# Kernel optimization log

Hardware: AMD Instinct MI355X
Metric: run time of the kernel (lower is better)

The kernel has to match this reference:

```python
import jax, jax.numpy as jnp
import numpy as np

B = 2048
D = 40960          # util.half_kp_numel(): 64 king squares * 640 piece-square planes
BASE = 288
MOVE = 4096        # util.move_numel(): 64 from-squares * 64 to-squares
MOVE_SIZE = (64, 64)


def setup_inputs() -> dict:
    key = jax.random.key(0)
    ks = jax.random.split(key, 24)
    f32 = jnp.float32
    # forward args: sparse one-hot half-kp occupancy vectors (modeled as rand floats)
    pov = (jax.random.uniform(ks[0], (B, 1), f32) > 0.5).astype(f32)
    white = (jax.random.uniform(ks[1], (B, D), f32) < 0.001).astype(f32)
    black = (jax.random.uniform(ks[2], (B, D), f32) < 0.001).astype(f32)
    s = 0.01
    p = {
        'W_w': jax.random.normal(ks[3], (BASE, D), f32) * s,
        'b_w': jnp.zeros((BASE,), f32),
        'W_b': jax.random.normal(ks[4], (BASE, D), f32) * s,
        'b_b': jnp.zeros((BASE,), f32),
        'W_v0': jax.random.normal(ks[5], (32, 2 * BASE), f32) * s,
        'b_v0': jnp.zeros((32,), f32),
        'W_v1': jax.random.normal(ks[6], (32, 32), f32) * s,
        'b_v1': jnp.zeros((32,), f32),
        'W_v2': jax.random.normal(ks[7], (1, 32), f32) * s,
        'b_v2': jnp.zeros((1,), f32),
        'W_a0': jax.random.normal(ks[8], (144, 2 * BASE), f32) * s,
        'b_a0': jnp.zeros((144,), f32),
        'W_a1': jax.random.normal(ks[9], (MOVE, 144), f32) * s,
        'b_a1': jnp.zeros((MOVE,), f32),
        'W_vs': jax.random.normal(ks[10], (1, 2 * BASE), f32) * s,
        'b_vs': jnp.zeros((1,), f32),
        'W_as': jax.random.normal(ks[11], (MOVE, 2 * BASE), f32) * s,
        'b_as': jnp.zeros((MOVE,), f32),
    }
    return dict(pov=pov, white=white, black=black, **p)


def _linear(x, W, b):
    return x @ W.T + b


def reference(pov, white, black, W_w, b_w, W_b, b_b,
              W_v0, b_v0, W_v1, b_v1, W_v2, b_v2,
              W_a0, b_a0, W_a1, b_a1, W_vs, b_vs, W_as, b_as):
    # half-kp affine accumulators (the sparse gather-sum candidate)
    w256 = _linear(white, W_w, b_w)            # [B, BASE]
    b256 = _linear(black, W_b, b_b)            # [B, BASE]
    cat_wb = jnp.concatenate([w256, b256], axis=1)
    cat_bw = jnp.concatenate([b256, w256], axis=1)
    base = jax.nn.relu(pov * cat_wb + (1.0 - pov) * cat_bw)  # [B, 2*BASE]
    # value head with skip
    val = jax.nn.relu(_linear(base, W_v0, b_v0))
    val = jax.nn.relu(_linear(val, W_v1, b_v1))
    val = _linear(val, W_v2, b_v2) + _linear(base, W_vs, b_vs)   # [B, 1]
    # action head with skip
    act = jax.nn.relu(_linear(base, W_a0, b_a0))
    act = _linear(act, W_a1, b_a1) + _linear(base, W_as, b_as)   # [B, MOVE]
    act = act.reshape(act.shape[0], *MOVE_SIZE)                  # [B, 64, 64]
    return (val, act)
```

## Files before the change

### kernel.cpp

```cpp
#include <hip/hip_runtime.h>

#define D_IN 40960
#define NB 2048
#define BASEN 288
#define CAPL 95
#define LSTRIDE 96
#define KP 736

typedef __attribute__((ext_vector_type(4))) float f32x4;
typedef __attribute__((ext_vector_type(8))) short short8;

__device__ inline float bf2f(ushort u) {
    unsigned v = ((unsigned)u) << 16; float f; __builtin_memcpy(&f, &v, 4); return f;
}
__device__ inline ushort f2bf(float f) {
    unsigned x; __builtin_memcpy(&x, &f, 4);
    unsigned r = (x + 0x7FFFu + ((x >> 16) & 1u)) >> 16; return (ushort)r;
}

__device__ inline void llds16(const void* g, void* l) {
    __builtin_amdgcn_global_load_lds((const __attribute__((address_space(1))) unsigned*)g,
                                     (__attribute__((address_space(3))) unsigned*)l, 16, 0, 0);
}

__global__ __launch_bounds__(256) void scan_kernel(const float* __restrict__ white,
                                                   const float* __restrict__ black,
                                                   int* __restrict__ lists) {
    int b = blockIdx.x, c = blockIdx.y;
    const float* src = (c ? black : white) + (size_t)b * D_IN;
    __shared__ int cnt;
    __shared__ int idxs[CAPL];
    if (threadIdx.x == 0) cnt = 0;
    __syncthreads();
    const uint4* v = (const uint4*)src;
    for (int it = 0; it < D_IN / (256 * 4); ++it) {
        int vi = it * 256 + threadIdx.x;
        uint4 x = v[vi];
        unsigned wds[4] = {x.x, x.y, x.z, x.w};
#pragma unroll
        for (int q = 0; q < 4; ++q) {
            if (wds[q]) { int p = atomicAdd(&cnt, 1); if (p < CAPL) idxs[p] = vi * 4 + q; }
        }
    }
    __syncthreads();
    int n = min(cnt, CAPL);
    int* dst = lists + ((size_t)c * NB + b) * LSTRIDE;
    if (threadIdx.x == 0) dst[0] = n;
    for (int i = threadIdx.x; i < n; i += 256) dst[1 + i] = idxs[i];
}

__global__ __launch_bounds__(256) void transpose_kernel(const float* __restrict__ src,
                                                        ushort* __restrict__ dst) {
    __shared__ float tile[32][65];
    int i = threadIdx.x;
    int d0 = blockIdx.x * 64, o0 = blockIdx.y * 32;
    int tr = i >> 4, tc4 = (i & 15) * 4;
#pragma unroll
    for (int rep = 0; rep < 2; ++rep) {
        int row = tr + rep * 16;
        float4 u = *(const float4*)&src[(size_t)(o0 + row) * D_IN + d0 + tc4];
        tile[row][tc4] = u.x; tile[row][tc4 + 1] = u.y; tile[row][tc4 + 2] = u.z; tile[row][tc4 + 3] = u.w;
    }
    __syncthreads();
    int dr = i >> 3, oc4 = (i & 7) * 4;
#pragma unroll
    for (int rep = 0; rep < 2; ++rep) {
        int d = dr + rep * 32;
        ushort4 u;
        u.x = f2bf(tile[oc4][d]); u.y = f2bf(tile[oc4 + 1][d]);
        u.z = f2bf(tile[oc4 + 2][d]); u.w = f2bf(tile[oc4 + 3][d]);
        *(ushort4*)&dst[(size_t)(d0 + d) * BASEN + o0 + oc4] = u;
    }
}

__global__ __launch_bounds__(288) void gatherW_kernel(const int* __restrict__ lists,
                                                      const ushort* __restrict__ Wt,
                                                      const float* __restrict__ b_w,
                                                      float* __restrict__ accW) {
    int b = blockIdx.x, t = threadIdx.x;
    __shared__ int idx[CAPL];
    __shared__ int ncnt;
    const int* lw = lists + (size_t)b * LSTRIDE;
    if (t == 0) ncnt = min(lw[0], CAPL);
    for (int i = t; i < CAPL; i += 288) idx[i] = lw[1 + i];
    __syncthreads();
    float acc = b_w[t];
    int n = ncnt;
#pragma unroll 4
    for (int i = 0; i < n; ++i) acc += bf2f(Wt[(size_t)idx[i] * BASEN + t]);
    accW[(size_t)b * BASEN + t] = acc;
}

__global__ __launch_bounds__(288) void gatherB_kernel(const int* __restrict__ lists,
                                                      const ushort* __restrict__ Wt,
                                                      const float* __restrict__ accW,
                                                      const float* __restrict__ pov,
                                                      const float* __restrict__ b_b,
                                                      const float* __restrict__ W_a0,
                                                      const float* __restrict__ b_a0,
                                                      ushort* __restrict__ hidden) {
    int b = blockIdx.x, t = threadIdx.x;
    __shared__ int idx[CAPL];
    __shared__ int ncnt;
    __shared__ float baseS[576];
    const int* lb = lists + ((size_t)NB + b) * LSTRIDE;
    if (t == 0) ncnt = min(lb[0], CAPL);
    for (int i = t; i < CAPL; i += 288) idx[i] = lb[1 + i];
    __syncthreads();
    float accB = b_b[t];
    int n = ncnt;
#pragma unroll 4
    for (int i = 0; i < n; ++i) accB += bf2f(Wt[(size_t)idx[i] * BASEN + t]);
    float aW = accW[(size_t)b * BASEN + t];
    float p = pov[b];
    float b0 = fmaxf(p * aW + (1.0f - p) * accB, 0.0f);
    float b1 = fmaxf(p * accB + (1.0f - p) * aW, 0.0f);
    baseS[t] = b0; baseS[288 + t] = b1;
    ushort* hrow = hidden + (size_t)b * KP;
    hrow[160 + t] = f2bf(b0);
    hrow[160 + 288 + t] = f2bf(b1);
    if (t < 16) hrow[144 + t] = 0;
    __syncthreads();
    int o = t >> 1, half = t & 1;
    const float* wrow = W_a0 + (size_t)o * 576 + half * 288;
    const float* bp = &baseS[half * 288];
    float s = 0.f;
#pragma unroll
    for (int j = 0; j < 288; j += 4) {
        float4 q = *(const float4*)(wrow + j);
        s += bp[j + 0] * q.x + bp[j + 1] * q.y + bp[j + 2] * q.z + bp[j + 3] * q.w;
    }
    s += __shfl_xor(s, 1);
    if (half == 0) hrow[o] = f2bf(fmaxf(s + b_a0[o], 0.f));
}

__global__ __launch_bounds__(256) void wcat_kernel(const float* __restrict__ W_a1,
                                                   const float* __restrict__ W_as,
                                                   const float* __restrict__ b_a1,
                                                   const float* __restrict__ b_as,
                                                   ushort* __restrict__ Wcat,
                                                   float* __restrict__ biasA) {
    int m = blockIdx.x, t = threadIdx.x;
    ushort* dst = Wcat + (size_t)m * KP;
    if (t < 144) dst[t] = f2bf(W_a1[(size_t)m * 144 + t]);
    if (t >= 144 && t < 160) dst[t] = 0;
    for (int j = t; j < 576; j += 256) dst[160 + j] = f2bf(W_as[(size_t)m * 576 + j]);
    if (t == 200) biasA[m] = b_a1[m] + b_as[m];
}

__global__ __launch_bounds__(64) void val_kernel(const ushort* __restrict__ hidden,
                                                 const float* __restrict__ W_v0, const float* __restrict__ b_v0,
                                                 const float* __restrict__ W_v1, const float* __restrict__ b_v1,
                                                 const float* __restrict__ W_v2, const float* __restrict__ b_v2,
                                                 const float* __restrict__ W_vs, const float* __restrict__ b_vs,
                                                 float* __restrict__ outv) {
    int b = blockIdx.x, t = threadIdx.x;
    __shared__ float bl[576];
    __shared__ float v0s[32];
    __shared__ float skipS;
    const ushort* hrow = hidden + (size_t)b * KP + 160;
    for (int i = t; i < 576; i += 64) bl[i] = bf2f(hrow[i]);
    __syncthreads();
    if (t < 32) {
        float s = b_v0[t];
        const float* w = W_v0 + (size_t)t * 576;
        for (int j = 0; j < 576; ++j) s += bl[j] * w[j];
        v0s[t] = fmaxf(s, 0.f);
    } else {
        int u = t - 32;
        float s = 0.f;
        for (int j = u; j < 576; j += 32) s += bl[j] * W_vs[j];
        s += __shfl_xor(s, 1); s += __shfl_xor(s, 2); s += __shfl_xor(s, 4);
        s += __shfl_xor(s, 8); s += __shfl_xor(s, 16);
        if (u == 0) skipS = s;
    }
    __syncthreads();
    if (t < 32) {
        float s = b_v1[t];
        const float* w = W_v1 + (size_t)t * 32;
        for (int j = 0; j < 32; ++j) s += v0s[j] * w[j];
        float v1t = fmaxf(s, 0.f);
        float part = v1t * W_v2[t];
        part += __shfl_xor(part, 1); part += __shfl_xor(part, 2); part += __shfl_xor(part, 4);
        part += __shfl_xor(part, 8); part += __shfl_xor(part, 16);
        if (t == 0) outv[b] = part + b_v2[0] + skipS + b_vs[0];
    }
}

__global__ __launch_bounds__(256) void gemm_act(const ushort* __restrict__ A,
                                                const ushort* __restrict__ Bm,
                                                const float* __restrict__ biasA,
                                                float* __restrict__ outa) {
    __shared__ ushort As[128 * 32];
    __shared__ ushort Bs[128 * 32];
    int tid = threadIdx.x;
    int lane = tid & 63, wv = tid >> 6;
    int bm = blockIdx.x, bn = blockIdx.y;
    int wm = wv & 1, wn = wv >> 1;
    f32x4 acc[4][4];
#pragma unroll
    for (int mt = 0; mt < 4; ++mt)
#pragma unroll
        for (int nt = 0; nt < 4; ++nt) { f32x4 z = {0.f, 0.f, 0.f, 0.f}; acc[mt][nt] = z; }

    int r = tid >> 2, c8 = (tid & 3) * 8;
    const ushort* Ag = A  + (size_t)(bm * 128 + r) * KP + c8;
    const ushort* Bg = Bm + (size_t)(bn * 128 + r) * KP + c8;
    ushort* AsW = As + wv * 512;
    ushort* BsW = Bs + wv * 512;

    int kg = (lane >> 4) * 8;
    int rA = wm * 64 + (lane & 15);
    int rB = wn * 64 + (lane & 15);

    for (int kk = 0; kk < KP; kk += 32) {
        llds16(Ag + kk, AsW);
        llds16(Ag + (size_t)64 * KP + kk, AsW + 2048);
        llds16(Bg + kk, BsW);
        llds16(Bg + (size_t)64 * KP + kk, BsW + 2048);
        __syncthreads();
        short8 af[4], bf[4];
#pragma unroll
        for (int mt = 0; mt < 4; ++mt) af[mt] = *(const short8*)&As[(rA + mt * 16) * 32 + kg];
#pragma unroll
        for (int nt = 0; nt < 4; ++nt) bf[nt] = *(const short8*)&Bs[(rB + nt * 16) * 32 + kg];
#pragma unroll
        for (int mt = 0; mt < 4; ++mt)
#pragma unroll
            for (int nt = 0; nt < 4; ++nt)
                acc[mt][nt] = __builtin_amdgcn_mfma_f32_16x16x32_bf16(af[mt], bf[nt], acc[mt][nt], 0, 0, 0);
        __syncthreads();
    }

    int colb = bn * 128 + wn * 64 + (lane & 15);
    int rowb = bm * 128 + wm * 64 + ((lane >> 4) << 2);
#pragma unroll
    for (int nt = 0; nt < 4; ++nt) {
        float bia = biasA[colb + nt * 16];
#pragma unroll
        for (int mt = 0; mt < 4; ++mt) {
#pragma unroll
            for (int q = 0; q < 4; ++q) {
                int rr = rowb + mt * 16 + q;
                outa[(size_t)rr * 4096 + colb + nt * 16] = acc[mt][nt][q] + bia;
            }
        }
    }
}

extern "C" void kernel_launch(void* const* d_in, const int* in_sizes, int n_in,
                              void* d_out, int out_size, void* d_ws, size_t ws_size,
                              hipStream_t stream) {
    const float* pov   = (const float*)d_in[0];
    const float* white = (const float*)d_in[1];
    const float* black = (const float*)d_in[2];
    const float* W_w   = (const float*)d_in[3];
    const float* b_w   = (const float*)d_in[4];
    const float* W_b   = (const float*)d_in[5];
    const float* b_b   = (const float*)d_in[6];
    const float* W_v0  = (const float*)d_in[7];
    const float* b_v0  = (const float*)d_in[8];
    const float* W_v1  = (const float*)d_in[9];
    const float* b_v1  = (const float*)d_in[10];
    const float* W_v2  = (const float*)d_in[11];
    const float* b_v2  = (const float*)d_in[12];
    const float* W_a0  = (const float*)d_in[13];
    const float* b_a0  = (const float*)d_in[14];
    const float* W_a1  = (const float*)d_in[15];
    const float* b_a1  = (const float*)d_in[16];
    const float* W_vs  = (const float*)d_in[17];
    const float* b_vs  = (const float*)d_in[18];
    const float* W_as  = (const float*)d_in[19];
    const float* b_as  = (const float*)d_in[20];

    char* ws = (char*)d_ws;
    ushort* Wtbuf = (ushort*)(ws + 0);
    ushort* Wcat  = (ushort*)(ws + 0);
    float*  biasA = (float*)(ws + 6029312);
    int*    lists = (int*)  (ws + 23592960);
    float*  accW  = (float*)(ws + 25165824);
    ushort* hidden= (ushort*)(ws + 27525120);

    float* outp = (float*)d_out;

    scan_kernel<<<dim3(NB, 2), 256, 0, stream>>>(white, black, lists);
    transpose_kernel<<<dim3(D_IN / 64, BASEN / 32), 256, 0, stream>>>(W_w, Wtbuf);
    gatherW_kernel<<<NB, 288, 0, stream>>>(lists, Wtbuf, b_w, accW);
    transpose_kernel<<<dim3(D_IN / 64, BASEN / 32), 256, 0, stream>>>(W_b, Wtbuf);
    gatherB_kernel<<<NB, 288, 0, stream>>>(lists, Wtbuf, accW, pov, b_b, W_a0, b_a0, hidden);
    wcat_kernel<<<4096, 256, 0, stream>>>(W_a1, W_as, b_a1, b_as, Wcat, biasA);
    val_kernel<<<NB, 64, 0, stream>>>(hidden, W_v0, b_v0, W_v1, b_v1, W_v2, b_v2, W_vs, b_vs, outp);
    gemm_act<<<dim3(2048 / 128, 4096 / 128), 256, 0, stream>>>(hidden, Wcat, biasA, outp + 2048);
}
```

Before: 927.7 us.

## Fuse scan, gathers, a0 and value head into one per-row kernel

Merges the occupancy scan, both half-kp gathers, the a0 hidden layer and the value head into a single 576-thread per-row kernel, so the index lists and the white accumulator no longer go through global memory. Both weight transposes now run in one launch, and W_a0 and W_v0 are converted to bf16 in a combined prep kernel. This cuts the launch count from eight to four and avoids intermediate global traffic. In exchange it needs separate transposed buffers for the two weight matrices, which enlarges the workspace, and the row kernel may run at lower occupancy.

New measurement: 871.8 us. -6.0%, faster.

```diff
diff --git a/kernel.cpp b/kernel.cpp
--- a/kernel.cpp
+++ b/kernel.cpp
@@ -4,7 +4,6 @@
 #define NB 2048
 #define BASEN 288
 #define CAPL 95
-#define LSTRIDE 96
 #define KP 736
 
 typedef __attribute__((ext_vector_type(4))) float f32x4;
@@ -23,34 +22,12 @@
                                      (__attribute__((address_space(3))) unsigned*)l, 16, 0, 0);
 }
 
-__global__ __launch_bounds__(256) void scan_kernel(const float* __restrict__ white,
-                                                   const float* __restrict__ black,
-                                                   int* __restrict__ lists) {
-    int b = blockIdx.x, c = blockIdx.y;
-    const float* src = (c ? black : white) + (size_t)b * D_IN;
-    __shared__ int cnt;
-    __shared__ int idxs[CAPL];
-    if (threadIdx.x == 0) cnt = 0;
-    __syncthreads();
-    const uint4* v = (const uint4*)src;
-    for (int it = 0; it < D_IN / (256 * 4); ++it) {
-        int vi = it * 256 + threadIdx.x;
-        uint4 x = v[vi];
-        unsigned wds[4] = {x.x, x.y, x.z, x.w};
-#pragma unroll
-        for (int q = 0; q < 4; ++q) {
-            if (wds[q]) { int p = atomicAdd(&cnt, 1); if (p < CAPL) idxs[p] = vi * 4 + q; }
-        }
-    }
-    __syncthreads();
-    int n = min(cnt, CAPL);
-    int* dst = lists + ((size_t)c * NB + b) * LSTRIDE;
-    if (threadIdx.x == 0) dst[0] = n;
-    for (int i = threadIdx.x; i < n; i += 256) dst[1 + i] = idxs[i];
-}
-
-__global__ __launch_bounds__(256) void transpose_kernel(const float* __restrict__ src,
-                                                        ushort* __restrict__ dst) {
+__global__ __launch_bounds__(256) void transpose_kernel(const float* __restrict__ Ww,
+                                                        const float* __restrict__ Wb,
+                                                        ushort* __restrict__ Wtw,
+                                                        ushort* __restrict__ Wtb) {
+    const float* src = blockIdx.z ? Wb : Ww;
+    ushort* dst = blockIdx.z ? Wtb : Wtw;
     __shared__ float tile[32][65];
     int i = threadIdx.x;
     int d0 = blockIdx.x * 64, o0 = blockIdx.y * 32;
@@ -73,114 +50,154 @@
     }
 }
 
-__global__ __launch_bounds__(288) void gatherW_kernel(const int* __restrict__ lists,
-                                                      const ushort* __restrict__ Wt,
-                                                      const float* __restrict__ b_w,
-                                                      float* __restrict__ accW) {
-    int b = blockIdx.x, t = threadIdx.x;
-    __shared__ int idx[CAPL];
-    __shared__ int ncnt;
-    const int* lw = lists + (size_t)b * LSTRIDE;
-    if (t == 0) ncnt = min(lw[0], CAPL);
-    for (int i = t; i < CAPL; i += 288) idx[i] = lw[1 + i];
-    __syncthreads();
-    float acc = b_w[t];
-    int n = ncnt;
-#pragma unroll 4
-    for (int i = 0; i < n; ++i) acc += bf2f(Wt[(size_t)idx[i] * BASEN + t]);
-    accW[(size_t)b * BASEN + t] = acc;
-}
-
-__global__ __launch_bounds__(288) void gatherB_kernel(const int* __restrict__ lists,
-                                                      const ushort* __restrict__ Wt,
-                                                      const float* __restrict__ accW,
-                                                      const float* __restrict__ pov,
-                                                      const float* __restrict__ b_b,
-                                                      const float* __restrict__ W_a0,
-                                                      const float* __restrict__ b_a0,
-                                                      ushort* __restrict__ hidden) {
-    int b = blockIdx.x, t = threadIdx.x;
-    __shared__ int idx[CAPL];
-    __shared__ int ncnt;
-    __shared__ float baseS[576];
-    const int* lb = lists + ((size_t)NB + b) * LSTRIDE;
-    if (t == 0) ncnt = min(lb[0], CAPL);
-    for (int i = t; i < CAPL; i += 288) idx[i] = lb[1 + i];
-    __syncthreads();
-    float accB = b_b[t];
-    int n = ncnt;
-#pragma unroll 4
-    for (int i = 0; i < n; ++i) accB += bf2f(Wt[(size_t)idx[i] * BASEN + t]);
-    float aW = accW[(size_t)b * BASEN + t];
-    float p = pov[b];
-    float b0 = fmaxf(p * aW + (1.0f - p) * accB, 0.0f);
-    float b1 = fmaxf(p * accB + (1.0f - p) * aW, 0.0f);
-    baseS[t] = b0; baseS[288 + t] = b1;
-    ushort* hrow = hidden + (size_t)b * KP;
-    hrow[160 + t] = f2bf(b0);
-    hrow[160 + 288 + t] = f2bf(b1);
-    if (t < 16) hrow[144 + t] = 0;
-    __syncthreads();
-    int o = t >> 1, half = t & 1;
-    const float* wrow = W_a0 + (size_t)o * 576 + half * 288;
-    const float* bp = &baseS[half * 288];
-    float s = 0.f;
-#pragma unroll
-    for (int j = 0; j < 288; j += 4) {
-        float4 q = *(const float4*)(wrow + j);
-        s += bp[j + 0] * q.x + bp[j + 1] * q.y + bp[j + 2] * q.z + bp[j + 3] * q.w;
-    }
-    s += __shfl_xor(s, 1);
-    if (half == 0) hrow[o] = f2bf(fmaxf(s + b_a0[o], 0.f));
-}
-
-__global__ __launch_bounds__(256) void wcat_kernel(const float* __restrict__ W_a1,
+__global__ __launch_bounds__(256) void prep_kernel(const float* __restrict__ W_a1,
                                                    const float* __restrict__ W_as,
                                                    const float* __restrict__ b_a1,
                                                    const float* __restrict__ b_as,
+                                                   const float* __restrict__ W_a0,
+                                                   const float* __restrict__ W_v0,
                                                    ushort* __restrict__ Wcat,
-                                                   float* __restrict__ biasA) {
+                                                   float* __restrict__ biasA,
+                                                   ushort* __restrict__ Wa0h,
+                                                   ushort* __restrict__ Wv0h) {
     int m = blockIdx.x, t = threadIdx.x;
-    ushort* dst = Wcat + (size_t)m * KP;
-    if (t < 144) dst[t] = f2bf(W_a1[(size_t)m * 144 + t]);
-    if (t >= 144 && t < 160) dst[t] = 0;
-    for (int j = t; j < 576; j += 256) dst[160 + j] = f2bf(W_as[(size_t)m * 576 + j]);
-    if (t == 200) biasA[m] = b_a1[m] + b_as[m];
-}
-
-__global__ __launch_bounds__(64) void val_kernel(const ushort* __restrict__ hidden,
-                                                 const float* __restrict__ W_v0, const float* __restrict__ b_v0,
-                                                 const float* __restrict__ W_v1, const float* __restrict__ b_v1,
-                                                 const float* __restrict__ W_v2, const float* __restrict__ b_v2,
-                                                 const float* __restrict__ W_vs, const float* __restrict__ b_vs,
-                                                 float* __restrict__ outv) {
+    if (m < 4096) {
+        ushort* dst = Wcat + (size_t)m * KP;
+        if (t < 144) dst[t] = f2bf(W_a1[(size_t)m * 144 + t]);
+        if (t >= 144 && t < 160) dst[t] = 0;
+        for (int j = t; j < 576; j += 256) dst[160 + j] = f2bf(W_as[(size_t)m * 576 + j]);
+        if (t == 200) biasA[m] = b_a1[m] + b_as[m];
+    } else if (m < 4096 + 144) {
+        int r = m - 4096;
+        for (int j = t; j < 576; j += 256) Wa0h[(size_t)r * 576 + j] = f2bf(W_a0[(size_t)r * 576 + j]);
+    } else {
+        int r = m - (4096 + 144);
+        for (int j = t; j < 576; j += 256) Wv0h[(size_t)r * 576 + j] = f2bf(W_v0[(size_t)r * 576 + j]);
+    }
+}
+
+__global__ __launch_bounds__(576) void row_kernel(const float* __restrict__ white,
+                                                  const float* __restrict__ black,
+                                                  const ushort* __restrict__ Wtw,
+                                                  const ushort* __restrict__ Wtb,
+                                                  const float* __restrict__ pov,
+                                                  const float* __restrict__ b_w,
+                                                  const float* __restrict__ b_b,
+                                                  const ushort* __restrict__ Wa0h,
+                                                  const float* __restrict__ b_a0,
+                                                  const ushort* __restrict__ Wv0h,
+                                                  const float* __restrict__ b_v0,
+                                                  const float* __restrict__ W_v1,
+                                                  const float* __restrict__ b_v1,
+                                                  const float* __restrict__ W_v2,
+                                                  const float* __restrict__ b_v2,
+                                                  const float* __restrict__ W_vs,
+                                                  const float* __restrict__ b_vs,
+                                                  ushort* __restrict__ hidden,
+                                                  float* __restrict__ outv) {
     int b = blockIdx.x, t = threadIdx.x;
-    __shared__ float bl[576];
+    __shared__ int cntW, cntB;
+    __shared__ int idxW[CAPL], idxB[CAPL];
+    __shared__ float accS[576];
+    __shared__ float baseS[576];
     __shared__ float v0s[32];
     __shared__ float skipS;
-    const ushort* hrow = hidden + (size_t)b * KP + 160;
-    for (int i = t; i < 576; i += 64) bl[i] = bf2f(hrow[i]);
-    __syncthreads();
-    if (t < 32) {
-        float s = b_v0[t];
-        const float* w = W_v0 + (size_t)t * 576;
-        for (int j = 0; j < 576; ++j) s += bl[j] * w[j];
-        v0s[t] = fmaxf(s, 0.f);
+    if (t == 0) cntW = 0;
+    if (t == 1) cntB = 0;
+    __syncthreads();
+
+    const uint4* vw = (const uint4*)(white + (size_t)b * D_IN);
+    const uint4* vb = (const uint4*)(black + (size_t)b * D_IN);
+    for (int i = t; i < D_IN / 4; i += 576) {
+        uint4 x = vw[i];
+        if (x.x) { int p = atomicAdd(&cntW, 1); if (p < CAPL) idxW[p] = i * 4; }
+        if (x.y) { int p = atomicAdd(&cntW, 1); if (p < CAPL) idxW[p] = i * 4 + 1; }
+        if (x.z) { int p = atomicAdd(&cntW, 1); if (p < CAPL) idxW[p] = i * 4 + 2; }
+        if (x.w) { int p = atomicAdd(&cntW, 1); if (p < CAPL) idxW[p] = i * 4 + 3; }
+        uint4 y = vb[i];
+        if (y.x) { int p = atomicAdd(&cntB, 1); if (p < CAPL) idxB[p] = i * 4; }
+        if (y.y) { int p = atomicAdd(&cntB, 1); if (p < CAPL) idxB[p] = i * 4 + 1; }
+        if (y.z) { int p = atomicAdd(&cntB, 1); if (p < CAPL) idxB[p] = i * 4 + 2; }
+        if (y.w) { int p = atomicAdd(&cntB, 1); if (p < CAPL) idxB[p] = i * 4 + 3; }
+    }
+    __syncthreads();
+
+    {
+        int col = (t < 288) ? t : t - 288;
+        const ushort* Wt = (t < 288) ? Wtw : Wtb;
+        const int* il = (t < 288) ? idxW : idxB;
+        int n = min((t < 288) ? cntW : cntB, CAPL);
+        float acc = (t < 288) ? b_w[col] : b_b[col];
+#pragma unroll 4
+        for (int i = 0; i < n; ++i) acc += bf2f(Wt[(size_t)il[i] * BASEN + col]);
+        accS[t] = acc;
+    }
+    __syncthreads();
+
+    float p = pov[b];
+    ushort* hrow = hidden + (size_t)b * KP;
+    if (t < 288) {
+        float aW = accS[t], aB = accS[288 + t];
+        float b0 = fmaxf(p * aW + (1.0f - p) * aB, 0.0f);
+        float b1 = fmaxf(p * aB + (1.0f - p) * aW, 0.0f);
+        baseS[t] = b0; baseS[288 + t] = b1;
+        hrow[160 + t] = f2bf(b0);
+        hrow[160 + 288 + t] = f2bf(b1);
+        if (t < 16) hrow[144 + t] = 0;
+    }
+    __syncthreads();
+
+    {
+        int o = t >> 2, q4 = t & 3;
+        const ushort* wr = Wa0h + (size_t)o * 576 + q4 * 144;
+        const float* bp = &baseS[q4 * 144];
+        float s = 0.f;
+#pragma unroll
+        for (int j = 0; j < 144; j += 8) {
+            uint4 q = *(const uint4*)(wr + j);
+            s += bp[j + 0] * bf2f((ushort)(q.x & 0xFFFF)) + bp[j + 1] * bf2f((ushort)(q.x >> 16))
+               + bp[j + 2] * bf2f((ushort)(q.y & 0xFFFF)) + bp[j + 3] * bf2f((ushort)(q.y >> 16))
+               + bp[j + 4] * bf2f((ushort)(q.z & 0xFFFF)) + bp[j + 5] * bf2f((ushort)(q.z >> 16))
+               + bp[j + 6] * bf2f((ushort)(q.w & 0xFFFF)) + bp[j + 7] * bf2f((ushort)(q.w >> 16));
+        }
+        s += __shfl_xor(s, 1);
+        s += __shfl_xor(s, 2);
+        if (q4 == 0) hrow[o] = f2bf(fmaxf(s + b_a0[o], 0.f));
+    }
+
+    if (t < 512) {
+        int o = t >> 4, sub = t & 15;
+        const ushort* wr = Wv0h + (size_t)o * 576 + sub * 36;
+        const float* bp = &baseS[sub * 36];
+        float s = 0.f;
+#pragma unroll
+        for (int j = 0; j < 36; j += 4) {
+            ushort4 q = *(const ushort4*)(wr + j);
+            s += bp[j + 0] * bf2f(q.x) + bp[j + 1] * bf2f(q.y)
+               + bp[j + 2] * bf2f(q.z) + bp[j + 3] * bf2f(q.w);
+        }
+        s += __shfl_xor(s, 1); s += __shfl_xor(s, 2);
+        s += __shfl_xor(s, 4); s += __shfl_xor(s, 8);
+        if (sub == 0) v0s[o] = fmaxf(s + b_v0[o], 0.f);
     } else {
-        int u = t - 32;
+        int u = t - 512;
+        const float* wp = W_vs + u * 9;
+        const float* bp = &baseS[u * 9];
         float s = 0.f;
-        for (int j = u; j < 576; j += 32) s += bl[j] * W_vs[j];
+#pragma unroll
+        for (int j = 0; j < 9; ++j) s += bp[j] * wp[j];
         s += __shfl_xor(s, 1); s += __shfl_xor(s, 2); s += __shfl_xor(s, 4);
-        s += __shfl_xor(s, 8); s += __shfl_xor(s, 16);
+        s += __shfl_xor(s, 8); s += __shfl_xor(s, 16); s += __shfl_xor(s, 32);
         if (u == 0) skipS = s;
     }
     __syncthreads();
+
     if (t < 32) {
         float s = b_v1[t];
         const float* w = W_v1 + (size_t)t * 32;
+#pragma unroll
         for (int j = 0; j < 32; ++j) s += v0s[j] * w[j];
-        float v1t = fmaxf(s, 0.f);
-        float part = v1t * W_v2[t];
+        float part = fmaxf(s, 0.f) * W_v2[t];
         part += __shfl_xor(part, 1); part += __shfl_xor(part, 2); part += __shfl_xor(part, 4);
         part += __shfl_xor(part, 8); part += __shfl_xor(part, 16);
         if (t == 0) outv[b] = part + b_v2[0] + skipS + b_vs[0];
@@ -274,21 +291,21 @@
     const float* b_as  = (const float*)d_in[20];
 
     char* ws = (char*)d_ws;
-    ushort* Wtbuf = (ushort*)(ws + 0);
-    ushort* Wcat  = (ushort*)(ws + 0);
-    float*  biasA = (float*)(ws + 6029312);
-    int*    lists = (int*)  (ws + 23592960);
-    float*  accW  = (float*)(ws + 25165824);
-    ushort* hidden= (ushort*)(ws + 27525120);
+    ushort* Wtw   = (ushort*)(ws + 0);
+    ushort* Wtb   = (ushort*)(ws + 23592960);
+    ushort* hidden= (ushort*)(ws + 47185920);
+    ushort* Wcat  = (ushort*)(ws + 50200576);
+    float*  biasA = (float*)(ws + 56229888);
+    ushort* Wa0h  = (ushort*)(ws + 56246272);
+    ushort* Wv0h  = (ushort*)(ws + 56412160);
 
     float* outp = (float*)d_out;
 
-    scan_kernel<<<dim3(NB, 2), 256, 0, stream>>>(white, black, lists);
-    transpose_kernel<<<dim3(D_IN / 64, BASEN / 32), 256, 0, stream>>>(W_w, Wtbuf);
-    gatherW_kernel<<<NB, 288, 0, stream>>>(lists, Wtbuf, b_w, accW);
-    transpose_kernel<<<dim3(D_IN / 64, BASEN / 32), 256, 0, stream>>>(W_b, Wtbuf);
-    gatherB_kernel<<<NB, 288, 0, stream>>>(lists, Wtbuf, accW, pov, b_b, W_a0, b_a0, hidden);
-    wcat_kernel<<<4096, 256, 0, stream>>>(W_a1, W_as, b_a1, b_as, Wcat, biasA);
-    val_kernel<<<NB, 64, 0, stream>>>(hidden, W_v0, b_v0, W_v1, b_v1, W_v2, b_v2, W_vs, b_vs, outp);
+    transpose_kernel<<<dim3(D_IN / 64, BASEN / 32, 2), 256, 0, stream>>>(W_w, W_b, Wtw, Wtb);
+    prep_kernel<<<4096 + 144 + 32, 256, 0, stream>>>(W_a1, W_as, b_a1, b_as, W_a0, W_v0,
+                                                     Wcat, biasA, Wa0h, Wv0h);
+    row_kernel<<<NB, 576, 0, stream>>>(white, black, Wtw, Wtb, pov, b_w, b_b,
+                                       Wa0h, b_a0, Wv0h, b_v0, W_v1, b_v1, W_v2, b_v2,
+                                       W_vs, b_vs, hidden, outp);
     gemm_act<<<dim3(2048 / 128, 4096 / 128), 256, 0, stream>>>(hidden, Wcat, biasA, outp + 2048);
 }
```
